# Optimization experiments

Measured on AMD Instinct MI355X. Metric: run time of the kernel, lower is better.

Reference implementation:

```python
import jax, jax.numpy as jnp
import numpy as np

DEPTH = 2
DIM = 64
INNER = 256  # hard-coded inner_dim in Attention
HEADS = 1
N = 4096
B = 2
EPS = 1e-5


def layernorm(x, g, b):
    m = jnp.mean(x, axis=-1, keepdims=True)
    v = jnp.var(x, axis=-1, keepdims=True)
    return (x - m) * jax.lax.rsqrt(v + EPS) * g + b


def setup_inputs() -> dict:
    key = jax.random.key(0)
    ks = jax.random.split(key, 16)
    embed = jax.random.normal(ks[0], (B, N, DIM), dtype=jnp.float32)
    A = jax.random.randint(ks[1], (1, HEADS, N, N), 0, 2).astype(jnp.float32)
    s = 0.02
    return {
        "embed": embed,
        "A": A,
        "g1": jnp.ones((DEPTH, DIM), jnp.float32),
        "b1": jnp.zeros((DEPTH, DIM), jnp.float32),
        "Wqkv": jax.random.normal(ks[2], (DEPTH, DIM, INNER * 3), jnp.float32) * s,
        "Wout": jax.random.normal(ks[3], (DEPTH, INNER, DIM), jnp.float32) * s,
        "bout": jnp.zeros((DEPTH, DIM), jnp.float32),
        "g2": jnp.ones((DEPTH, DIM), jnp.float32),
        "b2": jnp.zeros((DEPTH, DIM), jnp.float32),
        "W1": jax.random.normal(ks[4], (DEPTH, DIM, DIM), jnp.float32) * s,
        "bb1": jnp.zeros((DEPTH, DIM), jnp.float32),
        "W2": jax.random.normal(ks[5], (DEPTH, DIM, DIM), jnp.float32) * s,
        "bb2": jnp.zeros((DEPTH, DIM), jnp.float32),
        "gf": jnp.ones((DIM,), jnp.float32),
        "bf": jnp.zeros((DIM,), jnp.float32),
    }


def _encoder(embed, A, g1, b1, Wqkv, Wout, bout, g2, b2, W1, bb1, W2, bb2, gf, bf):
    b, n, dim = embed.shape
    scale = dim ** (-0.5)
    dh = INNER // HEADS
    x = embed
    attn = None
    dots_softmax = None
    diag = jnp.arange(n)
    for l in range(DEPTH):
        xn = layernorm(x, g1[l], b1[l])
        qkv = xn @ Wqkv[l]  # [b, n, 3*INNER]
        q, k, v = jnp.split(qkv, 3, axis=-1)
        # [b, n, INNER] -> [b, h, n, dh]
        q = q.reshape(b, n, HEADS, dh).transpose(0, 2, 1, 3)
        k = k.reshape(b, n, HEADS, dh).transpose(0, 2, 1, 3)
        v = v.reshape(b, n, HEADS, dh).transpose(0, 2, 1, 3)
        dots = jnp.einsum("bhid,bhjd->bhij", q, k) * scale
        dots_softmax = jax.nn.softmax(dots[0, 0], axis=-1)
        # adjacency mask, then only [0][0] kept; diagonal filled with literal 1.0;
        # the original does a cpu/numpy roundtrip with .detach() -> stop_gradient.
        e = jnp.where(A > 0, dots, jnp.float32(-9e15))[0, 0]  # [n, n]
        e = e.at[diag, diag].set(1.0)
        e = jax.lax.stop_gradient(e)
        attn = jax.nn.softmax(e, axis=-1)  # [n, n], shared across b, h
        out = jnp.einsum("ij,bhjd->bhid", attn, v)  # broadcast attn over b,h
        out = out.transpose(0, 2, 1, 3).reshape(b, n, INNER)
        out = out @ Wout[l] + bout[l]
        x = xn + out  # residual onto the NORMED input (as in original)
        xm = layernorm(x, g2[l], b2[l])
        mlp = jax.nn.gelu(xm @ W1[l] + bb1[l], approximate=False) @ W2[l] + bb2[l]
        x = xm + mlp
    x = layernorm(x, gf, bf)
    return x, attn.reshape(1, 1, n, n), dots_softmax


def reference(embed, A, g1, b1, Wqkv, Wout, bout, g2, b2, W1, bb1, W2, bb2, gf, bf):
    return _encoder(embed, A, g1, b1, Wqkv, Wout, bout, g2, b2, W1, bb1, W2, bb2, gf, bf)
```

## Files before the change

### kernel.cpp

```cpp
#include <hip/hip_runtime.h>
#include <hip/hip_bf16.h>
#include <math.h>

typedef __attribute__((ext_vector_type(8))) short short8;
typedef __attribute__((ext_vector_type(4))) float f32x4;

__device__ __forceinline__ unsigned short f2bf(float x) {
    __hip_bfloat16 b = __float2bfloat16(x);
    return *reinterpret_cast<unsigned short*>(&b);
}
__device__ __forceinline__ float gelu_exact(float x) {
    return 0.5f * x * (1.0f + erff(x * 0.70710678118654752f));
}

__global__ __launch_bounds__(256) void k_zero(float* __restrict__ p, long n)
{
    long i = (long)blockIdx.x * 256 + threadIdx.x;
    if (i < n) p[i] = 0.f;
}

__global__ __launch_bounds__(256) void k_layernorm(
    const float* __restrict__ x, const float* __restrict__ g,
    const float* __restrict__ b, float* __restrict__ out)
{
    int wave = threadIdx.x >> 6, lane = threadIdx.x & 63;
    long row = (long)blockIdx.x * 4 + wave;
    float v = x[row * 64 + lane];
    float s = v;
    #pragma unroll
    for (int o = 32; o; o >>= 1) s += __shfl_xor(s, o);
    float m = s * (1.0f / 64.0f);
    float d = v - m;
    float q = d * d;
    #pragma unroll
    for (int o = 32; o; o >>= 1) q += __shfl_xor(q, o);
    float rstd = rsqrtf(q * (1.0f / 64.0f) + 1e-5f);
    out[row * 64 + lane] = d * rstd * g[lane] + b[lane];
}

__global__ __launch_bounds__(256) void k_wfold(
    const float* __restrict__ Wqkv, const float* __restrict__ Wout,
    float* __restrict__ Wfold)
{
    int idx = blockIdx.x * 256 + threadIdx.x;
    int c = idx >> 6, d = idx & 63;
    float a = 0.f;
    for (int k = 0; k < 256; ++k)
        a += Wqkv[c * 768 + 512 + k] * Wout[k * 64 + d];
    Wfold[idx] = a;
}

__global__ __launch_bounds__(256) void k_maskpack(
    const float* __restrict__ Aadj, unsigned long long* __restrict__ mask)
{
    int row = blockIdx.x;
    int wave = threadIdx.x >> 6, lane = threadIdx.x & 63;
    for (int w = wave; w < 64; w += 4) {
        float a = Aadj[(long)row * 4096 + w * 64 + lane];
        unsigned long long m = __ballot(a > 0.f);
        if (lane == 0) mask[(long)row * 64 + w] = m;
    }
}

__global__ __launch_bounds__(256) void k_qk(
    const float* __restrict__ xn, const float* __restrict__ W,
    unsigned short* __restrict__ q, unsigned short* __restrict__ kmat)
{
    __shared__ float As[64][65];
    __shared__ float Ws[64][65];
    int tid = threadIdx.x;
    int m0 = blockIdx.x * 64, n0 = blockIdx.y * 64;
    #pragma unroll
    for (int it = 0; it < 16; ++it) {
        int idx = tid + it * 256;
        int r = idx >> 6, c = idx & 63;
        As[r][c] = xn[(long)(m0 + r) * 64 + c];
        Ws[r][c] = W[(long)r * 768 + n0 + c];
    }
    __syncthreads();
    int tx = tid & 15, ty = tid >> 4;
    float acc[4][4] = {};
    #pragma unroll
    for (int k = 0; k < 64; ++k) {
        float a[4], w[4];
        #pragma unroll
        for (int i = 0; i < 4; ++i) a[i] = As[ty * 4 + i][k];
        #pragma unroll
        for (int j = 0; j < 4; ++j) w[j] = Ws[k][tx * 4 + j];
        #pragma unroll
        for (int i = 0; i < 4; ++i)
            #pragma unroll
            for (int j = 0; j < 4; ++j) acc[i][j] += a[i] * w[j];
    }
    #pragma unroll
    for (int i = 0; i < 4; ++i) {
        long row = m0 + ty * 4 + i;
        #pragma unroll
        for (int j = 0; j < 4; ++j) {
            int col = n0 + tx * 4 + j;
            if (col < 256) q[row * 256 + col] = f2bf(acc[i][j]);
            else           kmat[row * 256 + (col - 256)] = f2bf(acc[i][j]);
        }
    }
}

__global__ __launch_bounds__(256) void k_xnw_t(
    const float* __restrict__ xn, const float* __restrict__ Wfold,
    unsigned short* __restrict__ vWT)
{
    __shared__ float As[64][65];
    __shared__ float Ws[64][65];
    int tid = threadIdx.x;
    int n0 = blockIdx.x * 64, b = blockIdx.y;
    #pragma unroll
    for (int it = 0; it < 16; ++it) {
        int idx = tid + it * 256;
        int r = idx >> 6, c = idx & 63;
        As[r][c] = xn[((long)b * 4096 + n0 + r) * 64 + c];
        Ws[r][c] = Wfold[r * 64 + c];
    }
    __syncthreads();
    int tx = tid & 15, ty = tid >> 4;
    float acc[4][4] = {};
    #pragma unroll
    for (int k = 0; k < 64; ++k) {
        float a[4], w[4];
        #pragma unroll
        for (int i = 0; i < 4; ++i) a[i] = As[ty * 4 + i][k];
        #pragma unroll
        for (int j = 0; j < 4; ++j) w[j] = Ws[k][tx * 4 + j];
        #pragma unroll
        for (int i = 0; i < 4; ++i)
            #pragma unroll
            for (int j = 0; j < 4; ++j) acc[i][j] += a[i] * w[j];
    }
    #pragma unroll
    for (int i = 0; i < 4; ++i)
        #pragma unroll
        for (int j = 0; j < 4; ++j)
            vWT[((long)b * 64 + tx * 4 + j) * 4096 + n0 + ty * 4 + i] = f2bf(acc[i][j]);
}

__global__ __launch_bounds__(256) void k_mfma_nt(
    const unsigned short* __restrict__ A, const unsigned short* __restrict__ B,
    float* __restrict__ C, int N, int K, float scale)
{
    __shared__ __align__(16) unsigned short As[128 * 64];
    __shared__ __align__(16) unsigned short Bs[128 * 64];
    int tid = threadIdx.x;
    int lane = tid & 63, wave = tid >> 6;
    long m0 = (long)blockIdx.x * 128, n0 = (long)blockIdx.y * 128;
    const unsigned short* Ag = A + m0 * K;
    const unsigned short* Bg = B + n0 * K;
    int wm = (wave & 1) * 64, wn = (wave >> 1) * 64;
    int fr = lane & 15, quad = lane >> 4;

    f32x4 acc[4][4];
    #pragma unroll
    for (int i = 0; i < 4; ++i)
        #pragma unroll
        for (int j = 0; j < 4; ++j) acc[i][j] = (f32x4){0.f, 0.f, 0.f, 0.f};

    for (int k0 = 0; k0 < K; k0 += 64) {
        #pragma unroll
        for (int it = 0; it < 4; ++it) {
            int c = tid + it * 256;
            int r = c >> 3, col = (c & 7) * 8;
            *(short8*)&As[c * 8] = *(const short8*)(Ag + (long)r * K + k0 + col);
            *(short8*)&Bs[c * 8] = *(const short8*)(Bg + (long)r * K + k0 + col);
        }
        __syncthreads();
        #pragma unroll
        for (int ks = 0; ks < 2; ++ks) {
            short8 af[4], bfr[4];
            #pragma unroll
            for (int i = 0; i < 4; ++i) {
                af[i]  = *(const short8*)&As[(wm + i * 16 + fr) * 64 + ks * 32 + quad * 8];
                bfr[i] = *(const short8*)&Bs[(wn + i * 16 + fr) * 64 + ks * 32 + quad * 8];
            }
            #pragma unroll
            for (int i = 0; i < 4; ++i)
                #pragma unroll
                for (int j = 0; j < 4; ++j)
                    acc[i][j] = __builtin_amdgcn_mfma_f32_16x16x32_bf16(
                        af[i], bfr[j], acc[i][j], 0, 0, 0);
        }
        __syncthreads();
    }
    #pragma unroll
    for (int i = 0; i < 4; ++i) {
        #pragma unroll
        for (int j = 0; j < 4; ++j) {
            long col = n0 + wn + j * 16 + fr;
            long rowb = m0 + wm + i * 16 + quad * 4;
            #pragma unroll
            for (int r = 0; r < 4; ++r)
                C[(rowb + r) * N + col] = acc[i][j][r] * scale;
        }
    }
}

__global__ __launch_bounds__(256) void k_mfma_splitk(
    const float* __restrict__ A, const unsigned short* __restrict__ B,
    float* __restrict__ C)
{
    __shared__ __align__(16) unsigned short As[128 * 64];
    __shared__ __align__(16) unsigned short Bs[128 * 64];
    const int K = 4096, N = 128;
    int tid = threadIdx.x;
    int lane = tid & 63, wave = tid >> 6;
    long m0 = (long)blockIdx.x * 128;
    int k0base = blockIdx.y * 512;
    const float* Ag = A + m0 * K;
    int wm = (wave & 1) * 64, wn = (wave >> 1) * 64;
    int fr = lane & 15, quad = lane >> 4;

    f32x4 acc[4][4];
    #pragma unroll
    for (int i = 0; i < 4; ++i)
        #pragma unroll
        for (int j = 0; j < 4; ++j) acc[i][j] = (f32x4){0.f, 0.f, 0.f, 0.f};

    for (int k0 = k0base; k0 < k0base + 512; k0 += 64) {
        #pragma unroll
        for (int it = 0; it < 4; ++it) {
            int c = tid + it * 256;
            int r = c >> 3, col = (c & 7) * 8;
            float4 f0 = *(const float4*)(Ag + (long)r * K + k0 + col);
            float4 f1 = *(const float4*)(Ag + (long)r * K + k0 + col + 4);
            short8 s;
            s[0] = (short)f2bf(f0.x); s[1] = (short)f2bf(f0.y);
            s[2] = (short)f2bf(f0.z); s[3] = (short)f2bf(f0.w);
            s[4] = (short)f2bf(f1.x); s[5] = (short)f2bf(f1.y);
            s[6] = (short)f2bf(f1.z); s[7] = (short)f2bf(f1.w);
            *(short8*)&As[c * 8] = s;
            *(short8*)&Bs[c * 8] = *(const short8*)(B + (long)r * K + k0 + col);
        }
        __syncthreads();
        #pragma unroll
        for (int ks = 0; ks < 2; ++ks) {
            short8 af[4], bfr[4];
            #pragma unroll
            for (int i = 0; i < 4; ++i) {
                af[i]  = *(const short8*)&As[(wm + i * 16 + fr) * 64 + ks * 32 + quad * 8];
                bfr[i] = *(const short8*)&Bs[(wn + i * 16 + fr) * 64 + ks * 32 + quad * 8];
            }
            #pragma unroll
            for (int i = 0; i < 4; ++i)
                #pragma unroll
                for (int j = 0; j < 4; ++j)
                    acc[i][j] = __builtin_amdgcn_mfma_f32_16x16x32_bf16(
                        af[i], bfr[j], acc[i][j], 0, 0, 0);
        }
        __syncthreads();
    }
    #pragma unroll
    for (int i = 0; i < 4; ++i) {
        #pragma unroll
        for (int j = 0; j < 4; ++j) {
            long col = wn + j * 16 + fr;
            long rowb = m0 + wm + i * 16 + quad * 4;
            #pragma unroll
            for (int r = 0; r < 4; ++r)
                atomicAdd(&C[(rowb + r) * N + col], acc[i][j][r]);
        }
    }
}

__device__ __forceinline__ float block_max(float v, float* red, int lane, int wave) {
    #pragma unroll
    for (int o = 32; o; o >>= 1) v = fmaxf(v, __shfl_xor(v, o));
    if (lane == 0) red[wave] = v;
    __syncthreads();
    v = fmaxf(fmaxf(red[0], red[1]), fmaxf(red[2], red[3]));
    __syncthreads();
    return v;
}
__device__ __forceinline__ float block_sum(float v, float* red, int lane, int wave) {
    #pragma unroll
    for (int o = 32; o; o >>= 1) v += __shfl_xor(v, o);
    if (lane == 0) red[wave] = v;
    __syncthreads();
    v = red[0] + red[1] + red[2] + red[3];
    __syncthreads();
    return v;
}

__global__ __launch_bounds__(256) void k_softmax_attn(
    float* __restrict__ dots, const float* __restrict__ Aadj,
    const unsigned long long* __restrict__ mask,
    float* __restrict__ attn_out, int write_ds)
{
    __shared__ float red[4];
    __shared__ unsigned long long msk[64];
    int row = blockIdx.x, tid = threadIdx.x;
    int lane = tid & 63, wave = tid >> 6;
    float* drow = dots + (long)row * 4096;
    if (mask) {
        if (tid < 64) msk[tid] = mask[(long)row * 64 + tid];
        __syncthreads();
    }
    float d[16], mv[16];
    float mmax = -1e30f, umax = -1e30f;
    #pragma unroll
    for (int i = 0; i < 16; ++i) {
        int j = tid + i * 256;
        float dv = drow[j];
        d[i] = dv;
        bool keep = mask ? ((msk[j >> 6] >> (j & 63)) & 1ull)
                         : (Aadj[(long)row * 4096 + j] > 0.f);
        float m = keep ? dv : -1e30f;
        if (j == row) m = 1.0f;
        mv[i] = m;
        mmax = fmaxf(mmax, m);
        umax = fmaxf(umax, dv);
    }
    float M1 = block_max(mmax, red, lane, wave);
    float s1 = 0.f;
    #pragma unroll
    for (int i = 0; i < 16; ++i) { float e = expf(mv[i] - M1); mv[i] = e; s1 += e; }
    s1 = block_sum(s1, red, lane, wave);
    float inv1 = 1.0f / s1;
    #pragma unroll
    for (int i = 0; i < 16; ++i)
        attn_out[(long)row * 4096 + tid + i * 256] = mv[i] * inv1;

    if (write_ds) {
        float M2 = block_max(umax, red, lane, wave);
        float s2 = 0.f;
        #pragma unroll
        for (int i = 0; i < 16; ++i) { float e = expf(d[i] - M2); d[i] = e; s2 += e; }
        s2 = block_sum(s2, red, lane, wave);
        float inv2 = 1.0f / s2;
        #pragma unroll
        for (int i = 0; i < 16; ++i)
            drow[tid + i * 256] = d[i] * inv2;
    }
}

__global__ __launch_bounds__(256) void k_avres(
    const float* __restrict__ xn, const float* __restrict__ avcat,
    const float* __restrict__ bout, float* __restrict__ x)
{
    int idx = blockIdx.x * 256 + threadIdx.x;
    int r = idx >> 6, c = idx & 63;
    int b = r >> 12, n = r & 4095;
    x[idx] = xn[idx] + avcat[(long)n * 128 + b * 64 + c] + bout[c];
}

__global__ __launch_bounds__(256) void k_gemm64(
    const float* __restrict__ A, const float* __restrict__ W,
    const float* __restrict__ bias, const float* __restrict__ res,
    float* __restrict__ out, int act)
{
    __shared__ float As[64][65];
    __shared__ float Ws[64][65];
    int tid = threadIdx.x;
    int m0 = blockIdx.x * 64;
    #pragma unroll
    for (int it = 0; it < 16; ++it) {
        int idx = tid + it * 256;
        int r = idx >> 6, c = idx & 63;
        As[r][c] = A[(long)(m0 + r) * 64 + c];
        Ws[r][c] = W[(long)r * 64 + c];
    }
    __syncthreads();
    int tx = tid & 15, ty = tid >> 4;
    float acc[4][4] = {};
    #pragma unroll
    for (int k = 0; k < 64; ++k) {
        float a[4], w[4];
        #pragma unroll
        for (int i = 0; i < 4; ++i) a[i] = As[ty * 4 + i][k];
        #pragma unroll
        for (int j = 0; j < 4; ++j) w[j] = Ws[k][tx * 4 + j];
        #pragma unroll
        for (int i = 0; i < 4; ++i)
            #pragma unroll
            for (int j = 0; j < 4; ++j) acc[i][j] += a[i] * w[j];
    }
    #pragma unroll
    for (int i = 0; i < 4; ++i) {
        long row = m0 + ty * 4 + i;
        #pragma unroll
        for (int j = 0; j < 4; ++j) {
            int col = tx * 4 + j;
            float v = acc[i][j] + bias[col];
            if (act) v = gelu_exact(v);
            if (res) v += res[row * 64 + col];
            out[row * 64 + col] = v;
        }
    }
}

extern "C" void kernel_launch(void* const* d_in, const int* in_sizes, int n_in,
                              void* d_out, int out_size, void* d_ws, size_t ws_size,
                              hipStream_t stream)
{
    const float* embed = (const float*)d_in[0];
    const float* Aadj  = (const float*)d_in[1];
    const float* g1    = (const float*)d_in[2];
    const float* b1    = (const float*)d_in[3];
    const float* Wqkv  = (const float*)d_in[4];
    const float* Wout  = (const float*)d_in[5];
    const float* bout  = (const float*)d_in[6];
    const float* g2    = (const float*)d_in[7];
    const float* b2    = (const float*)d_in[8];
    const float* W1    = (const float*)d_in[9];
    const float* bb1   = (const float*)d_in[10];
    const float* W2    = (const float*)d_in[11];
    const float* bb2   = (const float*)d_in[12];
    const float* gf    = (const float*)d_in[13];
    const float* bff   = (const float*)d_in[14];

    float* ox    = (float*)d_out;
    float* attnb = ox + 524288;
    float* dsb   = attnb + 16777216;

    if (ws_size < (10ull << 20)) {
        k_zero<<<133120, 256, 0, stream>>>(ox, 34078720l);
        return;
    }

    char* ws = (char*)d_ws;
    float*          x     = (float*)(ws + (0l << 20));
    float*          xn    = (float*)(ws + (2l << 20));
    float*          h     = (float*)(ws + (4l << 20));
    unsigned short* q     = (unsigned short*)(ws + (6l << 20));
    unsigned short* kmat  = (unsigned short*)(ws + (7l << 20));
    unsigned short* vwt   = (unsigned short*)(ws + (8l << 20));
    float*          Wfold = (float*)(ws + (9l << 20));
    unsigned long long* mask = (ws_size >= (12ull << 20))
        ? (unsigned long long*)(ws + (10l << 20)) : nullptr;

    if (mask) k_maskpack<<<4096, 256, 0, stream>>>(Aadj, mask);

    for (int l = 0; l < 2; ++l) {
        const float* Wq = Wqkv + (long)l * 64 * 768;
        k_layernorm<<<2048, 256, 0, stream>>>(l ? x : embed, g1 + 64 * l, b1 + 64 * l, xn);
        k_wfold<<<16, 256, 0, stream>>>(Wq, Wout + (long)l * 256 * 64, Wfold);
        k_qk<<<dim3(64, 8), 256, 0, stream>>>(xn, Wq, q, kmat);
        k_xnw_t<<<dim3(64, 2), 256, 0, stream>>>(xn, Wfold, vwt);
        k_mfma_nt<<<dim3(32, 32), 256, 0, stream>>>(q, kmat, dsb, 4096, 256, 0.125f);
        k_softmax_attn<<<4096, 256, 0, stream>>>(dsb, Aadj, mask, attnb, l == 1);
        k_zero<<<2048, 256, 0, stream>>>(ox, 524288l);
        k_mfma_splitk<<<dim3(32, 8), 256, 0, stream>>>(attnb, vwt, ox);
        k_avres<<<2048, 256, 0, stream>>>(xn, ox, bout + 64 * l, x);
        k_layernorm<<<2048, 256, 0, stream>>>(x, g2 + 64 * l, b2 + 64 * l, xn);
        k_gemm64<<<128, 256, 0, stream>>>(xn, W1 + (long)l * 4096, bb1 + 64 * l,
                                          nullptr, h, 1);
        k_gemm64<<<128, 256, 0, stream>>>(h, W2 + (long)l * 4096, bb2 + 64 * l,
                                          xn, x, 0);
    }
    k_layernorm<<<2048, 256, 0, stream>>>(x, gf, bff, ox);
}
```

Measured before the change: 524.5 us.

## Unroll layers, use bf16 intermediates in layer 0, fuse residual+LayerNorm and MLP

Unrolls the two layers in the host launcher and batches the Wfold computation for both layers into one launch. Layer 0, whose attention and scores are not outputs, now stores the score matrix and attention probabilities in bf16 through a new softmax kernel and a bf16-input split-K GEMM. The attention residual is fused with the following LayerNorm, and both MLP GEMMs, GELU, residual and the next LayerNorm go into a single kernel. The aim is to cut full-size N×N fp32 traffic and launch count, at the cost of bf16 rounding in layer 0's attention and some in-place buffer reuse (xn read and written by the same launch).

New measurement: 472.5 us. 9.9% less time.

```diff
diff --git a/kernel.cpp b/kernel.cpp
--- a/kernel.cpp
+++ b/kernel.cpp
@@ -8,6 +8,12 @@
 __device__ __forceinline__ unsigned short f2bf(float x) {
     __hip_bfloat16 b = __float2bfloat16(x);
     return *reinterpret_cast<unsigned short*>(&b);
+}
+__device__ __forceinline__ float bf2f(unsigned short u) {
+    unsigned int t = ((unsigned int)u) << 16;
+    float f;
+    __builtin_memcpy(&f, &t, 4);
+    return f;
 }
 __device__ __forceinline__ float gelu_exact(float x) {
     return 0.5f * x * (1.0f + erff(x * 0.70710678118654752f));
@@ -42,12 +48,15 @@
     const float* __restrict__ Wqkv, const float* __restrict__ Wout,
     float* __restrict__ Wfold)
 {
-    int idx = blockIdx.x * 256 + threadIdx.x;
+    int l = blockIdx.x >> 4;
+    int idx = (blockIdx.x & 15) * 256 + threadIdx.x;
     int c = idx >> 6, d = idx & 63;
+    const float* Wq = Wqkv + (long)l * 64 * 768;
+    const float* Wo = Wout + (long)l * 256 * 64;
     float a = 0.f;
     for (int k = 0; k < 256; ++k)
-        a += Wqkv[c * 768 + 512 + k] * Wout[k * 64 + d];
-    Wfold[idx] = a;
+        a += Wq[c * 768 + 512 + k] * Wo[k * 64 + d];
+    Wfold[l * 4096 + idx] = a;
 }
 
 __global__ __launch_bounds__(256) void k_maskpack(
@@ -143,7 +152,8 @@
 
 __global__ __launch_bounds__(256) void k_mfma_nt(
     const unsigned short* __restrict__ A, const unsigned short* __restrict__ B,
-    float* __restrict__ C, int N, int K, float scale)
+    float* __restrict__ C, unsigned short* __restrict__ Cb,
+    int N, int K, float scale)
 {
     __shared__ __align__(16) unsigned short As[128 * 64];
     __shared__ __align__(16) unsigned short Bs[128 * 64];
@@ -193,9 +203,15 @@
         for (int j = 0; j < 4; ++j) {
             long col = n0 + wn + j * 16 + fr;
             long rowb = m0 + wm + i * 16 + quad * 4;
-            #pragma unroll
-            for (int r = 0; r < 4; ++r)
-                C[(rowb + r) * N + col] = acc[i][j][r] * scale;
+            if (Cb) {
+                #pragma unroll
+                for (int r = 0; r < 4; ++r)
+                    Cb[(rowb + r) * N + col] = f2bf(acc[i][j][r] * scale);
+            } else {
+                #pragma unroll
+                for (int r = 0; r < 4; ++r)
+                    C[(rowb + r) * N + col] = acc[i][j][r] * scale;
+            }
         }
     }
 }
@@ -267,6 +283,66 @@
     }
 }
 
+__global__ __launch_bounds__(256) void k_mfma_splitk_b(
+    const unsigned short* __restrict__ A, const unsigned short* __restrict__ B,
+    float* __restrict__ C)
+{
+    __shared__ __align__(16) unsigned short As[128 * 64];
+    __shared__ __align__(16) unsigned short Bs[128 * 64];
+    const int K = 4096, N = 128;
+    int tid = threadIdx.x;
+    int lane = tid & 63, wave = tid >> 6;
+    long m0 = (long)blockIdx.x * 128;
+    int k0base = blockIdx.y * 512;
+    const unsigned short* Ag = A + m0 * K;
+    int wm = (wave & 1) * 64, wn = (wave >> 1) * 64;
+    int fr = lane & 15, quad = lane >> 4;
+
+    f32x4 acc[4][4];
+    #pragma unroll
+    for (int i = 0; i < 4; ++i)
+        #pragma unroll
+        for (int j = 0; j < 4; ++j) acc[i][j] = (f32x4){0.f, 0.f, 0.f, 0.f};
+
+    for (int k0 = k0base; k0 < k0base + 512; k0 += 64) {
+        #pragma unroll
+        for (int it = 0; it < 4; ++it) {
+            int c = tid + it * 256;
+            int r = c >> 3, col = (c & 7) * 8;
+            *(short8*)&As[c * 8] = *(const short8*)(Ag + (long)r * K + k0 + col);
+            *(short8*)&Bs[c * 8] = *(const short8*)(B + (long)r * K + k0 + col);
+        }
+        __syncthreads();
+        #pragma unroll
+        for (int ks = 0; ks < 2; ++ks) {
+            short8 af[4], bfr[4];
+            #pragma unroll
+            for (int i = 0; i < 4; ++i) {
+                af[i]  = *(const short8*)&As[(wm + i * 16 + fr) * 64 + ks * 32 + quad * 8];
+                bfr[i] = *(const short8*)&Bs[(wn + i * 16 + fr) * 64 + ks * 32 + quad * 8];
+            }
+            #pragma unroll
+            for (int i = 0; i < 4; ++i)
+                #pragma unroll
+                for (int j = 0; j < 4; ++j)
+                    acc[i][j] = __builtin_amdgcn_mfma_f32_16x16x32_bf16(
+                        af[i], bfr[j], acc[i][j], 0, 0, 0);
+        }
+        __syncthreads();
+    }
+    #pragma unroll
+    for (int i = 0; i < 4; ++i) {
+        #pragma unroll
+        for (int j = 0; j < 4; ++j) {
+            long col = wn + j * 16 + fr;
+            long rowb = m0 + wm + i * 16 + quad * 4;
+            #pragma unroll
+            for (int r = 0; r < 4; ++r)
+                atomicAdd(&C[(rowb + r) * N + col], acc[i][j][r]);
+        }
+    }
+}
+
 __device__ __forceinline__ float block_max(float v, float* red, int lane, int wave) {
     #pragma unroll
     for (int o = 32; o; o >>= 1) v = fmaxf(v, __shfl_xor(v, o));
@@ -338,31 +414,95 @@
     }
 }
 
-__global__ __launch_bounds__(256) void k_avres(
+__global__ __launch_bounds__(256) void k_softmax_b(
+    const unsigned short* __restrict__ dots, const float* __restrict__ Aadj,
+    const unsigned long long* __restrict__ mask,
+    unsigned short* __restrict__ attn_out)
+{
+    __shared__ float red[4];
+    __shared__ unsigned long long msk[64];
+    int row = blockIdx.x, tid = threadIdx.x;
+    int lane = tid & 63, wave = tid >> 6;
+    const unsigned short* drow = dots + (long)row * 4096 + tid * 16;
+    if (mask) {
+        if (tid < 64) msk[tid] = mask[(long)row * 64 + tid];
+        __syncthreads();
+    }
+    short8 dv0 = *(const short8*)drow;
+    short8 dv1 = *(const short8*)(drow + 8);
+    unsigned long long mword = mask ? msk[tid >> 2] : 0ull;
+    int bitbase = (tid & 3) * 16;
+    float mv[16];
+    float mmax = -1e30f;
+    #pragma unroll
+    for (int i = 0; i < 16; ++i) {
+        unsigned short u = (unsigned short)(i < 8 ? dv0[i] : dv1[i - 8]);
+        float dvf = bf2f(u);
+        int j = tid * 16 + i;
+        bool keep = mask ? ((mword >> (bitbase + i)) & 1ull)
+                         : (Aadj[(long)row * 4096 + j] > 0.f);
+        float m = keep ? dvf : -1e30f;
+        if (j == row) m = 1.0f;
+        mv[i] = m;
+        mmax = fmaxf(mmax, m);
+    }
+    float M1 = block_max(mmax, red, lane, wave);
+    float s1 = 0.f;
+    #pragma unroll
+    for (int i = 0; i < 16; ++i) { float e = expf(mv[i] - M1); mv[i] = e; s1 += e; }
+    s1 = block_sum(s1, red, lane, wave);
+    float inv1 = 1.0f / s1;
+    short8 o0, o1;
+    #pragma unroll
+    for (int i = 0; i < 8; ++i) {
+        o0[i] = (short)f2bf(mv[i] * inv1);
+        o1[i] = (short)f2bf(mv[i + 8] * inv1);
+    }
+    unsigned short* orow = attn_out + (long)row * 4096 + tid * 16;
+    *(short8*)orow = o0;
+    *(short8*)(orow + 8) = o1;
+}
+
+__global__ __launch_bounds__(256) void k_avres_ln(
     const float* __restrict__ xn, const float* __restrict__ avcat,
-    const float* __restrict__ bout, float* __restrict__ x)
-{
-    int idx = blockIdx.x * 256 + threadIdx.x;
-    int r = idx >> 6, c = idx & 63;
-    int b = r >> 12, n = r & 4095;
-    x[idx] = xn[idx] + avcat[(long)n * 128 + b * 64 + c] + bout[c];
-}
-
-__global__ __launch_bounds__(256) void k_gemm64(
-    const float* __restrict__ A, const float* __restrict__ W,
-    const float* __restrict__ bias, const float* __restrict__ res,
-    float* __restrict__ out, int act)
+    const float* __restrict__ bout, const float* __restrict__ g,
+    const float* __restrict__ b, float* __restrict__ out)
+{
+    int wave = threadIdx.x >> 6, lane = threadIdx.x & 63;
+    long row = (long)blockIdx.x * 4 + wave;
+    int bb = (int)(row >> 12), n = (int)(row & 4095);
+    float v = xn[row * 64 + lane] + avcat[(long)n * 128 + bb * 64 + lane] + bout[lane];
+    float s = v;
+    #pragma unroll
+    for (int o = 32; o; o >>= 1) s += __shfl_xor(s, o);
+    float m = s * (1.0f / 64.0f);
+    float d = v - m;
+    float q = d * d;
+    #pragma unroll
+    for (int o = 32; o; o >>= 1) q += __shfl_xor(q, o);
+    float rstd = rsqrtf(q * (1.0f / 64.0f) + 1e-5f);
+    out[row * 64 + lane] = d * rstd * g[lane] + b[lane];
+}
+
+__global__ __launch_bounds__(256) void k_mlp(
+    const float* __restrict__ xm,
+    const float* __restrict__ W1, const float* __restrict__ bb1,
+    const float* __restrict__ W2, const float* __restrict__ bb2,
+    const float* __restrict__ g, const float* __restrict__ b,
+    float* __restrict__ out)
 {
     __shared__ float As[64][65];
-    __shared__ float Ws[64][65];
+    __shared__ float W1s[64][65];
+    __shared__ float W2s[64][65];
     int tid = threadIdx.x;
     int m0 = blockIdx.x * 64;
     #pragma unroll
     for (int it = 0; it < 16; ++it) {
         int idx = tid + it * 256;
         int r = idx >> 6, c = idx & 63;
-        As[r][c] = A[(long)(m0 + r) * 64 + c];
-        Ws[r][c] = W[(long)r * 64 + c];
+        As[r][c]  = xm[(long)(m0 + r) * 64 + c];
+        W1s[r][c] = W1[(long)r * 64 + c];
+        W2s[r][c] = W2[(long)r * 64 + c];
     }
     __syncthreads();
     int tx = tid & 15, ty = tid >> 4;
@@ -373,22 +513,55 @@
         #pragma unroll
         for (int i = 0; i < 4; ++i) a[i] = As[ty * 4 + i][k];
         #pragma unroll
-        for (int j = 0; j < 4; ++j) w[j] = Ws[k][tx * 4 + j];
+        for (int j = 0; j < 4; ++j) w[j] = W1s[k][tx * 4 + j];
         #pragma unroll
         for (int i = 0; i < 4; ++i)
             #pragma unroll
             for (int j = 0; j < 4; ++j) acc[i][j] += a[i] * w[j];
     }
+    __syncthreads();
+    #pragma unroll
+    for (int i = 0; i < 4; ++i)
+        #pragma unroll
+        for (int j = 0; j < 4; ++j)
+            W1s[ty * 4 + i][tx * 4 + j] = gelu_exact(acc[i][j] + bb1[tx * 4 + j]);
+    __syncthreads();
+    float acc2[4][4] = {};
+    #pragma unroll
+    for (int k = 0; k < 64; ++k) {
+        float a[4], w[4];
+        #pragma unroll
+        for (int i = 0; i < 4; ++i) a[i] = W1s[ty * 4 + i][k];
+        #pragma unroll
+        for (int j = 0; j < 4; ++j) w[j] = W2s[k][tx * 4 + j];
+        #pragma unroll
+        for (int i = 0; i < 4; ++i)
+            #pragma unroll
+            for (int j = 0; j < 4; ++j) acc2[i][j] += a[i] * w[j];
+    }
     #pragma unroll
     for (int i = 0; i < 4; ++i) {
+        float v[4];
+        float s = 0.f;
+        #pragma unroll
+        for (int j = 0; j < 4; ++j) {
+            v[j] = acc2[i][j] + bb2[tx * 4 + j] + As[ty * 4 + i][tx * 4 + j];
+            s += v[j];
+        }
+        #pragma unroll
+        for (int o = 1; o < 16; o <<= 1) s += __shfl_xor(s, o);
+        float m = s * (1.0f / 64.0f);
+        float q = 0.f;
+        #pragma unroll
+        for (int j = 0; j < 4; ++j) { float d = v[j] - m; q += d * d; }
+        #pragma unroll
+        for (int o = 1; o < 16; o <<= 1) q += __shfl_xor(q, o);
+        float rstd = rsqrtf(q * (1.0f / 64.0f) + 1e-5f);
         long row = m0 + ty * 4 + i;
         #pragma unroll
         for (int j = 0; j < 4; ++j) {
             int col = tx * 4 + j;
-            float v = acc[i][j] + bias[col];
-            if (act) v = gelu_exact(v);
-            if (res) v += res[row * 64 + col];
-            out[row * 64 + col] = v;
+            out[row * 64 + col] = (v[j] - m) * rstd * g[col] + b[col];
         }
     }
 }
@@ -432,25 +605,32 @@
     float*          Wfold = (float*)(ws + (9l << 20));
     unsigned long long* mask = (ws_size >= (12ull << 20))
         ? (unsigned long long*)(ws + (10l << 20)) : nullptr;
+    (void)x; (void)h;
+
+    unsigned short* dots_b = (unsigned short*)dsb;
+    unsigned short* attn_b = (unsigned short*)attnb;
 
     if (mask) k_maskpack<<<4096, 256, 0, stream>>>(Aadj, mask);
-
-    for (int l = 0; l < 2; ++l) {
-        const float* Wq = Wqkv + (long)l * 64 * 768;
-        k_layernorm<<<2048, 256, 0, stream>>>(l ? x : embed, g1 + 64 * l, b1 + 64 * l, xn);
-        k_wfold<<<16, 256, 0, stream>>>(Wq, Wout + (long)l * 256 * 64, Wfold);
-        k_qk<<<dim3(64, 8), 256, 0, stream>>>(xn, Wq, q, kmat);
-        k_xnw_t<<<dim3(64, 2), 256, 0, stream>>>(xn, Wfold, vwt);
-        k_mfma_nt<<<dim3(32, 32), 256, 0, stream>>>(q, kmat, dsb, 4096, 256, 0.125f);
-        k_softmax_attn<<<4096, 256, 0, stream>>>(dsb, Aadj, mask, attnb, l == 1);
-        k_zero<<<2048, 256, 0, stream>>>(ox, 524288l);
-        k_mfma_splitk<<<dim3(32, 8), 256, 0, stream>>>(attnb, vwt, ox);
-        k_avres<<<2048, 256, 0, stream>>>(xn, ox, bout + 64 * l, x);
-        k_layernorm<<<2048, 256, 0, stream>>>(x, g2 + 64 * l, b2 + 64 * l, xn);
-        k_gemm64<<<128, 256, 0, stream>>>(xn, W1 + (long)l * 4096, bb1 + 64 * l,
-                                          nullptr, h, 1);
-        k_gemm64<<<128, 256, 0, stream>>>(h, W2 + (long)l * 4096, bb2 + 64 * l,
-                                          xn, x, 0);
-    }
-    k_layernorm<<<2048, 256, 0, stream>>>(x, gf, bff, ox);
-}
+    k_wfold<<<32, 256, 0, stream>>>(Wqkv, Wout, Wfold);
+
+    k_layernorm<<<2048, 256, 0, stream>>>(embed, g1, b1, xn);
+    k_qk<<<dim3(64, 8), 256, 0, stream>>>(xn, Wqkv, q, kmat);
+    k_xnw_t<<<dim3(64, 2), 256, 0, stream>>>(xn, Wfold, vwt);
+    k_mfma_nt<<<dim3(32, 32), 256, 0, stream>>>(q, kmat, nullptr, dots_b, 4096, 256, 0.125f);
+    k_softmax_b<<<4096, 256, 0, stream>>>(dots_b, Aadj, mask, attn_b);
+    k_zero<<<2048, 256, 0, stream>>>(ox, 524288l);
+    k_mfma_splitk_b<<<dim3(32, 8), 256, 0, stream>>>(attn_b, vwt, ox);
+    k_avres_ln<<<2048, 256, 0, stream>>>(xn, ox, bout, g2, b2, xn);
+    k_mlp<<<128, 256, 0, stream>>>(xn, W1, bb1, W2, bb2,
+                                   g1 + 64, b1 + 64, xn);
+
+    k_qk<<<dim3(64, 8), 256, 0, stream>>>(xn, Wqkv + 64 * 768, q, kmat);
+    k_xnw_t<<<dim3(64, 2), 256, 0, stream>>>(xn, Wfold + 4096, vwt);
+    k_mfma_nt<<<dim3(32, 32), 256, 0, stream>>>(q, kmat, dsb, nullptr, 4096, 256, 0.125f);
+    k_softmax_attn<<<4096, 256, 0, stream>>>(dsb, Aadj, mask, attnb, 1);
+    k_zero<<<2048, 256, 0, stream>>>(ox, 524288l);
+    k_mfma_splitk<<<dim3(32, 8), 256, 0, stream>>>(attnb, vwt, ox);
+    k_avres_ln<<<2048, 256, 0, stream>>>(xn, ox, bout + 64, g2 + 64, b2 + 64, xn);
+    k_mlp<<<128, 256, 0, stream>>>(xn, W1 + 4096, bb1 + 64, W2 + 4096, bb2 + 64,
+                                   gf, bff, ox);
+}
```
